# Kernel tuning notes

Hardware: AMD Instinct MI355X
Metric: run time of the kernel (lower is better)

The kernel has to match this reference:

```python
import jax, jax.numpy as jnp
import numpy as np

N, M, D = 20000, 16000, 128

def setup_inputs() -> dict:
    key = jax.random.key(0)
    ks = jax.random.split(key, 4)
    return {
        "clear_feature": jax.random.normal(ks[0], (N, D), dtype=jnp.float32),
        "rain_feature": jax.random.normal(ks[1], (M, D), dtype=jnp.float32),
        # torch nn.Linear weight layout: (out_features, in_features)
        "W1": jax.random.normal(ks[2], (D, 2 * D), dtype=jnp.float32) * 0.05,
        "b1": jnp.zeros((D,), dtype=jnp.float32),
        "W2": jax.random.normal(ks[3], (1, D), dtype=jnp.float32) * 0.05,
        "b2": jnp.zeros((1,), dtype=jnp.float32),
    }

def reference(clear_feature, rain_feature, W1, b1, W2, b2):
    # --- KNN alignment (k=1): argmin of squared Euclidean distance == cdist+topk(smallest) ---
    x2 = jnp.sum(clear_feature * clear_feature, axis=-1, keepdims=True)   # [N,1]
    y2 = jnp.sum(rain_feature * rain_feature, axis=-1)                    # [M]
    d2 = x2 + y2 - 2.0 * (clear_feature @ rain_feature.T)                 # [N,M]
    idx = jnp.argmin(d2, axis=-1)                                         # [N]
    aligned = rain_feature[idx]                                           # [N,D] gather
    # --- attention MLP: Linear(2D->D) + ReLU + Linear(D->1) + Sigmoid ---
    comb = jnp.concatenate([clear_feature, aligned], axis=-1)             # [N,2D]
    h = jax.nn.relu(comb @ W1.T + b1)                                     # [N,D]
    w = jax.nn.sigmoid(h @ W2.T + b2)                                     # [N,1]
    # --- gated fusion ---
    return w * clear_feature + (1.0 - w) * aligned
```

## Files before the change

### kernel.cpp

```cpp
#include <hip/hip_runtime.h>
#include <stdint.h>

#define NN 20000
#define MM 16000
#define DD 128
#define CT2 250
#define SPLITS 32
#define RB2 40

typedef unsigned long long u64;
typedef _Float16 f16x8 __attribute__((ext_vector_type(8)));
typedef float f32x16 __attribute__((ext_vector_type(16)));

__global__ void k_y2(const float* __restrict__ rain, float* __restrict__ y2) {
    int row = blockIdx.x * 4 + (threadIdx.x >> 6);
    int lane = threadIdx.x & 63;
    if (row >= MM) return;
    float2 v = ((const float2*)(rain + (size_t)row * DD))[lane];
    float s = v.x * v.x + v.y * v.y;
    #pragma unroll
    for (int off = 32; off > 0; off >>= 1) s += __shfl_down(s, off);
    if (lane == 0) y2[row] = s;
}

__global__ void k_split_B(const float* __restrict__ rain, _Float16* __restrict__ Bimg) {
    int id = blockIdx.x * 256 + threadIdx.x;
    if (id >= CT2 * 1024) return;
    int cl = id & 31;
    int cg = (id >> 5) & 1;
    int kp = (id >> 6) & 15;
    int tc = id >> 10;
    int row = tc * 64 + cg * 32 + cl;
    const float4* src = (const float4*)(rain + (size_t)row * DD + kp * 8);
    float4 v0 = src[0], v1 = src[1];
    float x[8] = {v0.x, v0.y, v0.z, v0.w, v1.x, v1.y, v1.z, v1.w};
    _Float16 hi[8], lo[8];
    #pragma unroll
    for (int j = 0; j < 8; ++j) {
        _Float16 h = (_Float16)x[j];
        hi[j] = h;
        lo[j] = (_Float16)(x[j] - (float)h);
    }
    int ks = kp >> 1, kh = kp & 1;
    int chunk = ((ks * 2 + cg) * 2 + kh) * 32 + cl;
    size_t base = (size_t)tc * 16384;
    *(f16x8*)(Bimg + base + (size_t)chunk * 8) = *(f16x8*)hi;
    *(f16x8*)(Bimg + base + 8192 + (size_t)chunk * 8) = *(f16x8*)lo;
}

__global__ void k_w1img(const float* __restrict__ W1, _Float16* __restrict__ W1img) {
    int id = blockIdx.x * 256 + threadIdx.x;
    if (id >= 4096) return;
    int cl = id & 31;
    int kh = (id >> 5) & 1;
    int cg = (id >> 6) & 3;
    int ks = id >> 8;
    int d = cg * 32 + cl;
    int k = ks * 16 + kh * 8;
    const float4* src = (const float4*)(W1 + (size_t)d * 256 + k);
    float4 v0 = src[0], v1 = src[1];
    float x[8] = {v0.x, v0.y, v0.z, v0.w, v1.x, v1.y, v1.z, v1.w};
    _Float16 h[8];
    #pragma unroll
    for (int j = 0; j < 8; ++j) h[j] = (_Float16)x[j];
    *(f16x8*)(W1img + (size_t)id * 8) = *(f16x8*)h;
}

__global__ __launch_bounds__(512, 2) void k_dist(
        const float* __restrict__ clear_f,
        const _Float16* __restrict__ Bimg, const float* __restrict__ y2,
        u64* __restrict__ keys2) {
    __shared__ _Float16 lds[3][16384];
    __shared__ float y2s[512];

    const int tid = threadIdx.x;
    const int w = tid >> 6, lane = tid & 63;
    const int l5 = lane >> 5, l31 = lane & 31;
    const int b = blockIdx.x;
    const int split = b & 31;
    const int n0 = (b >> 5) * 512;
    const int nt = (CT2 - split + SPLITS - 1) / SPLITS;

    #define STAGE(T, BUF) do {                                                 \
        const _Float16* gsrc_ = Bimg + (size_t)(T) * 16384;                    \
        _Float16* dst_ = &lds[BUF][0];                                         \
        _Pragma("unroll")                                                      \
        for (int n_ = 0; n_ < 4; ++n_) {                                       \
            int seg_ = w * 4 + n_;                                             \
            __builtin_amdgcn_global_load_lds(                                  \
                (const __attribute__((address_space(1))) unsigned int*)        \
                    (gsrc_ + (size_t)seg_ * 512 + (size_t)lane * 8),           \
                (__attribute__((address_space(3))) unsigned int*)              \
                    (dst_ + (size_t)seg_ * 512),                               \
                16, 0, 0);                                                     \
        }                                                                      \
    } while (0)

    STAGE(split, 0);
    if (nt > 1) STAGE(split + SPLITS, 1);

    for (int j = tid; j < nt * 64; j += 512) {
        int tt = j >> 6;
        int cc = j & 63;
        y2s[j] = y2[(split + tt * SPLITS) * 64 + cc];
    }

    f16x8 afh[2][8], afl[2][8];
    #pragma unroll
    for (int rb = 0; rb < 2; ++rb) {
        int r = n0 + w * 64 + rb * 32 + l31;
        if (r >= NN) r = NN - 1;
        const float* ap = clear_f + (size_t)r * DD + l5 * 8;
        #pragma unroll
        for (int ks = 0; ks < 8; ++ks) {
            float4 v0 = *(const float4*)(ap + ks * 16);
            float4 v1 = *(const float4*)(ap + ks * 16 + 4);
            float x[8] = {v0.x, v0.y, v0.z, v0.w, v1.x, v1.y, v1.z, v1.w};
            _Float16 hi[8], lo[8];
            #pragma unroll
            for (int j = 0; j < 8; ++j) {
                float s = -2.f * x[j];
                _Float16 h = (_Float16)s;
                hi[j] = h;
                lo[j] = (_Float16)(s - (float)h);
            }
            afh[rb][ks] = *(f16x8*)hi;
            afl[rb][ks] = *(f16x8*)lo;
        }
    }

    asm volatile("s_waitcnt lgkmcnt(0)" ::: "memory");

    float bestd[32];
    unsigned bits[4] = {0u, 0u, 0u, 0u};
    #pragma unroll
    for (int s = 0; s < 32; ++s) bestd[s] = 1e30f;

    int p = 0;
    for (int i = 0; i < nt; ++i) {
        if (i + 1 < nt) {
            asm volatile("s_waitcnt vmcnt(4)" ::: "memory");
        } else {
            asm volatile("s_waitcnt vmcnt(0)" ::: "memory");
        }
        __builtin_amdgcn_s_barrier();
        __builtin_amdgcn_sched_barrier(0);

        if (i + 2 < nt) {
            int p2 = p + 2; if (p2 >= 3) p2 -= 3;
            STAGE(split + (i + 2) * SPLITS, p2);
        }

        float y2v0 = y2s[i * 64 + l31];
        float y2v1 = y2s[i * 64 + 32 + l31];

        f32x16 acc00, acc01, acc10, acc11;
        #pragma unroll
        for (int e = 0; e < 16; ++e) {
            acc00[e] = y2v0; acc10[e] = y2v0;
            acc01[e] = y2v1; acc11[e] = y2v1;
        }

        const _Float16* lbuf = &lds[p][0];
        #pragma unroll
        for (int ks = 0; ks < 8; ++ks) {
            f16x8 bh0 = *(const f16x8*)(lbuf + (size_t)(ks * 2 + 0) * 512 + (size_t)lane * 8);
            f16x8 bh1 = *(const f16x8*)(lbuf + (size_t)(ks * 2 + 1) * 512 + (size_t)lane * 8);
            f16x8 bl0 = *(const f16x8*)(lbuf + 8192 + (size_t)(ks * 2 + 0) * 512 + (size_t)lane * 8);
            f16x8 bl1 = *(const f16x8*)(lbuf + 8192 + (size_t)(ks * 2 + 1) * 512 + (size_t)lane * 8);
            __builtin_amdgcn_s_setprio(1);
            acc00 = __builtin_amdgcn_mfma_f32_32x32x16_f16(afh[0][ks], bh0, acc00, 0, 0, 0);
            acc10 = __builtin_amdgcn_mfma_f32_32x32x16_f16(afh[1][ks], bh0, acc10, 0, 0, 0);
            acc01 = __builtin_amdgcn_mfma_f32_32x32x16_f16(afh[0][ks], bh1, acc01, 0, 0, 0);
            acc11 = __builtin_amdgcn_mfma_f32_32x32x16_f16(afh[1][ks], bh1, acc11, 0, 0, 0);
            acc00 = __builtin_amdgcn_mfma_f32_32x32x16_f16(afh[0][ks], bl0, acc00, 0, 0, 0);
            acc10 = __builtin_amdgcn_mfma_f32_32x32x16_f16(afh[1][ks], bl0, acc10, 0, 0, 0);
            acc01 = __builtin_amdgcn_mfma_f32_32x32x16_f16(afh[0][ks], bl1, acc01, 0, 0, 0);
            acc11 = __builtin_amdgcn_mfma_f32_32x32x16_f16(afh[1][ks], bl1, acc11, 0, 0, 0);
            acc00 = __builtin_amdgcn_mfma_f32_32x32x16_f16(afl[0][ks], bh0, acc00, 0, 0, 0);
            acc10 = __builtin_amdgcn_mfma_f32_32x32x16_f16(afl[1][ks], bh0, acc10, 0, 0, 0);
            acc01 = __builtin_amdgcn_mfma_f32_32x32x16_f16(afl[0][ks], bh1, acc01, 0, 0, 0);
            acc11 = __builtin_amdgcn_mfma_f32_32x32x16_f16(afl[1][ks], bh1, acc11, 0, 0, 0);
            __builtin_amdgcn_s_setprio(0);
        }

        const unsigned ibase = (unsigned)i << 1;
        #pragma unroll
        for (int e = 0; e < 16; ++e) {
            {
                float d0 = acc00[e], d1 = acc01[e];
                bool tk = d1 < d0;
                float dm = tk ? d1 : d0;
                int s = e, sh = 4 * (e & 7);
                bool up = dm < bestd[s];
                bestd[s] = up ? dm : bestd[s];
                unsigned nib = ibase | (unsigned)tk;
                bits[s >> 3] = up ? ((bits[s >> 3] & ~(15u << sh)) | (nib << sh))
                                  : bits[s >> 3];
            }
            {
                float d0 = acc10[e], d1 = acc11[e];
                bool tk = d1 < d0;
                float dm = tk ? d1 : d0;
                int s = 16 + e, sh = 4 * (s & 7);
                bool up = dm < bestd[s];
                bestd[s] = up ? dm : bestd[s];
                unsigned nib = ibase | (unsigned)tk;
                bits[s >> 3] = up ? ((bits[s >> 3] & ~(15u << sh)) | (nib << sh))
                                  : bits[s >> 3];
            }
        }

        ++p; if (p == 3) p = 0;
    }
    #undef STAGE

    #pragma unroll
    for (int s = 0; s < 32; ++s) {
        unsigned nib = (bits[s >> 3] >> (4 * (s & 7))) & 15u;
        int i4 = (int)(nib >> 1), cg = (int)(nib & 1);
        int col = (split + i4 * SPLITS) * 64 + cg * 32 + l31;
        unsigned u = __float_as_uint(bestd[s]);
        u = (u & 0x80000000u) ? ~u : (u | 0x80000000u);
        u64 key = ((u64)u << 32) | (unsigned)col;
        #pragma unroll
        for (int off = 1; off < 32; off <<= 1) {
            u64 o = __shfl_xor(key, off);
            if (o < key) key = o;
        }
        if (l31 == 0) {
            int e = s & 15, rb = s >> 4;
            int grow = n0 + w * 64 + rb * 32 + (e & 3) + 8 * (e >> 2) + 4 * l5;
            if (grow < NN) keys2[(size_t)grow * SPLITS + split] = key;
        }
    }
}

__global__ void k_reduce(const u64* __restrict__ keys2, int* __restrict__ idx) {
    int gid = blockIdx.x * 256 + threadIdx.x;
    int row = gid >> 5, j = gid & 31;
    if (row >= NN) return;
    u64 k = keys2[(size_t)row * SPLITS + j];
    #pragma unroll
    for (int off = 16; off > 0; off >>= 1) {
        u64 o = __shfl_xor(k, off);
        if (o < k) k = o;
    }
    if (j == 0) idx[row] = (int)(k & 0xffffffffu);
}

__global__ __launch_bounds__(64) void k_mlp(
        const float* __restrict__ clear_f, const float* __restrict__ rain_f,
        const _Float16* __restrict__ W1img, const float* __restrict__ b1,
        const float* __restrict__ W2, const float* __restrict__ b2,
        const int* __restrict__ idx, float* __restrict__ out) {
    const int lane = threadIdx.x;
    const int l5 = lane >> 5, l31 = lane & 31;
    const int n0 = blockIdx.x * 32;

    int n = n0 + l31;
    int nc = n < NN ? n : NN - 1;
    int rid = idx[nc];
    f16x8 af[16];
    #pragma unroll
    for (int ks = 0; ks < 16; ++ks) {
        int k0 = ks * 16 + l5 * 8;
        const float4* src = (k0 < 128)
            ? (const float4*)(clear_f + (size_t)nc * DD + k0)
            : (const float4*)(rain_f + (size_t)rid * DD + (k0 - 128));
        float4 v0 = src[0], v1 = src[1];
        float x[8] = {v0.x, v0.y, v0.z, v0.w, v1.x, v1.y, v1.z, v1.w};
        _Float16 h[8];
        #pragma unroll
        for (int j = 0; j < 8; ++j) h[j] = (_Float16)x[j];
        af[ks] = *(f16x8*)h;
    }

    f32x16 acc[4];
    #pragma unroll
    for (int cg = 0; cg < 4; ++cg)
        #pragma unroll
        for (int e = 0; e < 16; ++e) acc[cg][e] = 0.f;

    #pragma unroll
    for (int ks = 0; ks < 16; ++ks) {
        #pragma unroll
        for (int cg = 0; cg < 4; ++cg) {
            f16x8 bh = *(const f16x8*)(W1img +
                ((size_t)((ks * 4 + cg) * 2 + l5)) * 256 + (size_t)l31 * 8);
            acc[cg] = __builtin_amdgcn_mfma_f32_32x32x16_f16(af[ks], bh, acc[cg], 0, 0, 0);
        }
    }

    float b1v[4], w2v[4];
    #pragma unroll
    for (int cg = 0; cg < 4; ++cg) {
        b1v[cg] = b1[cg * 32 + l31];
        w2v[cg] = W2[cg * 32 + l31];
    }
    float b2v = b2[0];

    #pragma unroll
    for (int e = 0; e < 16; ++e) {
        float part = 0.f;
        #pragma unroll
        for (int cg = 0; cg < 4; ++cg) {
            float hv = acc[cg][e] + b1v[cg];
            hv = hv > 0.f ? hv : 0.f;
            part = fmaf(hv, w2v[cg], part);
        }
        #pragma unroll
        for (int off = 1; off < 32; off <<= 1) part += __shfl_xor(part, off);
        float s = part + b2v;
        float wv = 1.f / (1.f + expf(-s));
        int row = n0 + (e & 3) + 8 * (e >> 2) + 4 * l5;
        if (row < NN) {
            int rid2 = idx[row];
            float4 cv = *(const float4*)(clear_f + (size_t)row * DD + l31 * 4);
            float4 av = *(const float4*)(rain_f + (size_t)rid2 * DD + l31 * 4);
            float4 ov;
            ov.x = wv * cv.x + (1.f - wv) * av.x;
            ov.y = wv * cv.y + (1.f - wv) * av.y;
            ov.z = wv * cv.z + (1.f - wv) * av.z;
            ov.w = wv * cv.w + (1.f - wv) * av.w;
            *(float4*)(out + (size_t)row * DD + l31 * 4) = ov;
        }
    }
}

extern "C" void kernel_launch(void* const* d_in, const int* in_sizes, int n_in,
                              void* d_out, int out_size, void* d_ws, size_t ws_size,
                              hipStream_t stream) {
    const float* clear_f = (const float*)d_in[0];
    const float* rain_f = (const float*)d_in[1];
    const float* W1 = (const float*)d_in[2];
    const float* b1 = (const float*)d_in[3];
    const float* W2 = (const float*)d_in[4];
    const float* b2 = (const float*)d_in[5];
    float* out = (float*)d_out;

    char* ws = (char*)d_ws;
    u64* keys2 = (u64*)ws;
    int* idx = (int*)(ws + 5120000);
    float* y2 = (float*)(ws + 5200000);
    _Float16* Bimg = (_Float16*)(ws + 5264000);
    _Float16* W1img = (_Float16*)(ws + 13456000);

    k_y2<<<MM / 4, 256, 0, stream>>>(rain_f, y2);
    k_split_B<<<(CT2 * 1024 + 255) / 256, 256, 0, stream>>>(rain_f, Bimg);
    k_w1img<<<16, 256, 0, stream>>>(W1, W1img);
    k_dist<<<RB2 * SPLITS, 512, 0, stream>>>(clear_f, Bimg, y2, keys2);
    k_reduce<<<(NN * 32 + 255) / 256, 256, 0, stream>>>(keys2, idx);
    k_mlp<<<(NN + 31) / 32, 64, 0, stream>>>(clear_f, rain_f, W1img, b1, W2, b2, idx, out);
}
```

Baseline: 414.4 us.

## Shrink distance tile to 32x32 per wave with double-buffered LDS

Reworks the KNN distance kernel so each wave computes a 32-row by 32-column tile instead of 64x64. Blocks drop to 256 threads with 128 rows each, launched over many more row blocks. The B image is repacked into 32-column tiles, the triple-buffered async pipeline becomes a double buffer synchronised with __syncthreads, and the lo-correction term gets its own accumulator. The aim is more occupancy and more blocks in flight, at the cost of less register and LDS reuse per MFMA, a full barrier every iteration, and a dependent MFMA chain on the main accumulator.

After: 357.3 us. 13.8% less time.

```diff
diff --git a/kernel.cpp b/kernel.cpp
--- a/kernel.cpp
+++ b/kernel.cpp
@@ -4,9 +4,9 @@
 #define NN 20000
 #define MM 16000
 #define DD 128
-#define CT2 250
+#define CT 500
 #define SPLITS 32
-#define RB2 40
+#define RBG 157
 
 typedef unsigned long long u64;
 typedef _Float16 f16x8 __attribute__((ext_vector_type(8)));
@@ -25,13 +25,13 @@
 
 __global__ void k_split_B(const float* __restrict__ rain, _Float16* __restrict__ Bimg) {
     int id = blockIdx.x * 256 + threadIdx.x;
-    if (id >= CT2 * 1024) return;
+    if (id >= CT * 512) return;
     int cl = id & 31;
-    int cg = (id >> 5) & 1;
-    int kp = (id >> 6) & 15;
-    int tc = id >> 10;
-    int row = tc * 64 + cg * 32 + cl;
-    const float4* src = (const float4*)(rain + (size_t)row * DD + kp * 8);
+    int kh = (id >> 5) & 1;
+    int ks = (id >> 6) & 7;
+    int tc = id >> 9;
+    int m = tc * 32 + cl;
+    const float4* src = (const float4*)(rain + (size_t)m * DD + ks * 16 + kh * 8);
     float4 v0 = src[0], v1 = src[1];
     float x[8] = {v0.x, v0.y, v0.z, v0.w, v1.x, v1.y, v1.z, v1.w};
     _Float16 hi[8], lo[8];
@@ -41,11 +41,10 @@
         hi[j] = h;
         lo[j] = (_Float16)(x[j] - (float)h);
     }
-    int ks = kp >> 1, kh = kp & 1;
-    int chunk = ((ks * 2 + cg) * 2 + kh) * 32 + cl;
-    size_t base = (size_t)tc * 16384;
+    int chunk = (ks * 2 + kh) * 32 + cl;
+    size_t base = (size_t)tc * 8192;
     *(f16x8*)(Bimg + base + (size_t)chunk * 8) = *(f16x8*)hi;
-    *(f16x8*)(Bimg + base + 8192 + (size_t)chunk * 8) = *(f16x8*)lo;
+    *(f16x8*)(Bimg + base + 4096 + (size_t)chunk * 8) = *(f16x8*)lo;
 }
 
 __global__ void k_w1img(const float* __restrict__ W1, _Float16* __restrict__ W1img) {
@@ -66,11 +65,11 @@
     *(f16x8*)(W1img + (size_t)id * 8) = *(f16x8*)h;
 }
 
-__global__ __launch_bounds__(512, 2) void k_dist(
+__global__ __launch_bounds__(256, 3) void k_dist(
         const float* __restrict__ clear_f,
         const _Float16* __restrict__ Bimg, const float* __restrict__ y2,
         u64* __restrict__ keys2) {
-    __shared__ _Float16 lds[3][16384];
+    __shared__ _Float16 lds[2][8192];
     __shared__ float y2s[512];
 
     const int tid = threadIdx.x;
@@ -78,11 +77,11 @@
     const int l5 = lane >> 5, l31 = lane & 31;
     const int b = blockIdx.x;
     const int split = b & 31;
-    const int n0 = (b >> 5) * 512;
-    const int nt = (CT2 - split + SPLITS - 1) / SPLITS;
+    const int n0 = (b >> 5) * 128;
+    const int nt = (CT - split + SPLITS - 1) / SPLITS;
 
     #define STAGE(T, BUF) do {                                                 \
-        const _Float16* gsrc_ = Bimg + (size_t)(T) * 16384;                    \
+        const _Float16* gsrc_ = Bimg + (size_t)(T) * 8192;                     \
         _Float16* dst_ = &lds[BUF][0];                                         \
         _Pragma("unroll")                                                      \
         for (int n_ = 0; n_ < 4; ++n_) {                                       \
@@ -97,18 +96,16 @@
     } while (0)
 
     STAGE(split, 0);
-    if (nt > 1) STAGE(split + SPLITS, 1);
-
-    for (int j = tid; j < nt * 64; j += 512) {
-        int tt = j >> 6;
-        int cc = j & 63;
-        y2s[j] = y2[(split + tt * SPLITS) * 64 + cc];
-    }
-
-    f16x8 afh[2][8], afl[2][8];
-    #pragma unroll
-    for (int rb = 0; rb < 2; ++rb) {
-        int r = n0 + w * 64 + rb * 32 + l31;
+
+    for (int j = tid; j < nt * 32; j += 256) {
+        int tt = j >> 5;
+        int cc = j & 31;
+        y2s[j] = y2[(split + tt * SPLITS) * 32 + cc];
+    }
+
+    f16x8 afh[8], afl[8];
+    {
+        int r = n0 + w * 32 + l31;
         if (r >= NN) r = NN - 1;
         const float* ap = clear_f + (size_t)r * DD + l5 * 8;
         #pragma unroll
@@ -124,102 +121,60 @@
                 hi[j] = h;
                 lo[j] = (_Float16)(s - (float)h);
             }
-            afh[rb][ks] = *(f16x8*)hi;
-            afl[rb][ks] = *(f16x8*)lo;
-        }
-    }
-
-    asm volatile("s_waitcnt lgkmcnt(0)" ::: "memory");
-
-    float bestd[32];
-    unsigned bits[4] = {0u, 0u, 0u, 0u};
-    #pragma unroll
-    for (int s = 0; s < 32; ++s) bestd[s] = 1e30f;
+            afh[ks] = *(f16x8*)hi;
+            afl[ks] = *(f16x8*)lo;
+        }
+    }
+
+    __syncthreads();
+
+    float bestd[16];
+    unsigned bits[2] = {0u, 0u};
+    #pragma unroll
+    for (int s = 0; s < 16; ++s) bestd[s] = 1e30f;
 
     int p = 0;
     for (int i = 0; i < nt; ++i) {
-        if (i + 1 < nt) {
-            asm volatile("s_waitcnt vmcnt(4)" ::: "memory");
-        } else {
-            asm volatile("s_waitcnt vmcnt(0)" ::: "memory");
-        }
-        __builtin_amdgcn_s_barrier();
-        __builtin_amdgcn_sched_barrier(0);
-
-        if (i + 2 < nt) {
-            int p2 = p + 2; if (p2 >= 3) p2 -= 3;
-            STAGE(split + (i + 2) * SPLITS, p2);
-        }
-
-        float y2v0 = y2s[i * 64 + l31];
-        float y2v1 = y2s[i * 64 + 32 + l31];
-
-        f32x16 acc00, acc01, acc10, acc11;
+        if (i + 1 < nt) STAGE(split + (i + 1) * SPLITS, 1 - p);
+
+        float y2v = y2s[i * 32 + l31];
+
+        f32x16 accA, accB;
+        #pragma unroll
+        for (int e = 0; e < 16; ++e) { accA[e] = y2v; accB[e] = 0.f; }
+
+        const _Float16* lbuf = &lds[p][0];
+        #pragma unroll
+        for (int ks = 0; ks < 8; ++ks) {
+            f16x8 bh = *(const f16x8*)(lbuf + (size_t)ks * 512 + (size_t)lane * 8);
+            f16x8 bl = *(const f16x8*)(lbuf + 4096 + (size_t)ks * 512 + (size_t)lane * 8);
+            __builtin_amdgcn_s_setprio(1);
+            accA = __builtin_amdgcn_mfma_f32_32x32x16_f16(afh[ks], bh, accA, 0, 0, 0);
+            accB = __builtin_amdgcn_mfma_f32_32x32x16_f16(afl[ks], bh, accB, 0, 0, 0);
+            accA = __builtin_amdgcn_mfma_f32_32x32x16_f16(afh[ks], bl, accA, 0, 0, 0);
+            __builtin_amdgcn_s_setprio(0);
+        }
+
+        const unsigned nib = (unsigned)i;
         #pragma unroll
         for (int e = 0; e < 16; ++e) {
-            acc00[e] = y2v0; acc10[e] = y2v0;
-            acc01[e] = y2v1; acc11[e] = y2v1;
-        }
-
-        const _Float16* lbuf = &lds[p][0];
-        #pragma unroll
-        for (int ks = 0; ks < 8; ++ks) {
-            f16x8 bh0 = *(const f16x8*)(lbuf + (size_t)(ks * 2 + 0) * 512 + (size_t)lane * 8);
-            f16x8 bh1 = *(const f16x8*)(lbuf + (size_t)(ks * 2 + 1) * 512 + (size_t)lane * 8);
-            f16x8 bl0 = *(const f16x8*)(lbuf + 8192 + (size_t)(ks * 2 + 0) * 512 + (size_t)lane * 8);
-            f16x8 bl1 = *(const f16x8*)(lbuf + 8192 + (size_t)(ks * 2 + 1) * 512 + (size_t)lane * 8);
-            __builtin_amdgcn_s_setprio(1);
-            acc00 = __builtin_amdgcn_mfma_f32_32x32x16_f16(afh[0][ks], bh0, acc00, 0, 0, 0);
-            acc10 = __builtin_amdgcn_mfma_f32_32x32x16_f16(afh[1][ks], bh0, acc10, 0, 0, 0);
-            acc01 = __builtin_amdgcn_mfma_f32_32x32x16_f16(afh[0][ks], bh1, acc01, 0, 0, 0);
-            acc11 = __builtin_amdgcn_mfma_f32_32x32x16_f16(afh[1][ks], bh1, acc11, 0, 0, 0);
-            acc00 = __builtin_amdgcn_mfma_f32_32x32x16_f16(afh[0][ks], bl0, acc00, 0, 0, 0);
-            acc10 = __builtin_amdgcn_mfma_f32_32x32x16_f16(afh[1][ks], bl0, acc10, 0, 0, 0);
-            acc01 = __builtin_amdgcn_mfma_f32_32x32x16_f16(afh[0][ks], bl1, acc01, 0, 0, 0);
-            acc11 = __builtin_amdgcn_mfma_f32_32x32x16_f16(afh[1][ks], bl1, acc11, 0, 0, 0);
-            acc00 = __builtin_amdgcn_mfma_f32_32x32x16_f16(afl[0][ks], bh0, acc00, 0, 0, 0);
-            acc10 = __builtin_amdgcn_mfma_f32_32x32x16_f16(afl[1][ks], bh0, acc10, 0, 0, 0);
-            acc01 = __builtin_amdgcn_mfma_f32_32x32x16_f16(afl[0][ks], bh1, acc01, 0, 0, 0);
-            acc11 = __builtin_amdgcn_mfma_f32_32x32x16_f16(afl[1][ks], bh1, acc11, 0, 0, 0);
-            __builtin_amdgcn_s_setprio(0);
-        }
-
-        const unsigned ibase = (unsigned)i << 1;
-        #pragma unroll
-        for (int e = 0; e < 16; ++e) {
-            {
-                float d0 = acc00[e], d1 = acc01[e];
-                bool tk = d1 < d0;
-                float dm = tk ? d1 : d0;
-                int s = e, sh = 4 * (e & 7);
-                bool up = dm < bestd[s];
-                bestd[s] = up ? dm : bestd[s];
-                unsigned nib = ibase | (unsigned)tk;
-                bits[s >> 3] = up ? ((bits[s >> 3] & ~(15u << sh)) | (nib << sh))
-                                  : bits[s >> 3];
-            }
-            {
-                float d0 = acc10[e], d1 = acc11[e];
-                bool tk = d1 < d0;
-                float dm = tk ? d1 : d0;
-                int s = 16 + e, sh = 4 * (s & 7);
-                bool up = dm < bestd[s];
-                bestd[s] = up ? dm : bestd[s];
-                unsigned nib = ibase | (unsigned)tk;
-                bits[s >> 3] = up ? ((bits[s >> 3] & ~(15u << sh)) | (nib << sh))
-                                  : bits[s >> 3];
-            }
-        }
-
-        ++p; if (p == 3) p = 0;
+            float d = accA[e] + accB[e];
+            int sh = 4 * (e & 7);
+            bool up = d < bestd[e];
+            bestd[e] = up ? d : bestd[e];
+            bits[e >> 3] = up ? ((bits[e >> 3] & ~(15u << sh)) | (nib << sh))
+                              : bits[e >> 3];
+        }
+
+        __syncthreads();
+        p ^= 1;
     }
     #undef STAGE
 
     #pragma unroll
-    for (int s = 0; s < 32; ++s) {
+    for (int s = 0; s < 16; ++s) {
         unsigned nib = (bits[s >> 3] >> (4 * (s & 7))) & 15u;
-        int i4 = (int)(nib >> 1), cg = (int)(nib & 1);
-        int col = (split + i4 * SPLITS) * 64 + cg * 32 + l31;
+        int col = (split + (int)nib * SPLITS) * 32 + l31;
         unsigned u = __float_as_uint(bestd[s]);
         u = (u & 0x80000000u) ? ~u : (u | 0x80000000u);
         u64 key = ((u64)u << 32) | (unsigned)col;
@@ -229,8 +184,7 @@
             if (o < key) key = o;
         }
         if (l31 == 0) {
-            int e = s & 15, rb = s >> 4;
-            int grow = n0 + w * 64 + rb * 32 + (e & 3) + 8 * (e >> 2) + 4 * l5;
+            int grow = n0 + w * 32 + (s & 3) + 8 * (s >> 2) + 4 * l5;
             if (grow < NN) keys2[(size_t)grow * SPLITS + split] = key;
         }
     }
@@ -347,9 +301,9 @@
     _Float16* W1img = (_Float16*)(ws + 13456000);
 
     k_y2<<<MM / 4, 256, 0, stream>>>(rain_f, y2);
-    k_split_B<<<(CT2 * 1024 + 255) / 256, 256, 0, stream>>>(rain_f, Bimg);
+    k_split_B<<<(CT * 512 + 255) / 256, 256, 0, stream>>>(rain_f, Bimg);
     k_w1img<<<16, 256, 0, stream>>>(W1, W1img);
-    k_dist<<<RB2 * SPLITS, 512, 0, stream>>>(clear_f, Bimg, y2, keys2);
+    k_dist<<<RBG * SPLITS, 256, 0, stream>>>(clear_f, Bimg, y2, keys2);
     k_reduce<<<(NN * 32 + 255) / 256, 256, 0, stream>>>(keys2, idx);
     k_mlp<<<(NN + 31) / 32, 64, 0, stream>>>(clear_f, rain_f, W1img, b1, W2, b2, idx, out);
 }
```

## Fuse prep kernels, shrink dist blocks, software-pipeline argmin fold, fold reduce into MLP

Applied to the files above, without the earlier changes.

The three preprocessing kernels merge into one launch, and the separate reduce kernel is folded into the MLP kernel, which now min-reduces the split keys itself. The distance kernel drops from 512-thread blocks with triple buffering to 256-thread blocks with double buffering and more blocks. Its inner loop splits into two column halves so the argmin fold of one half can overlap the MFMAs of the other. This targets launch overhead and ALU/MFMA serialization, at the cost of a full __syncthreads per tile and less prefetch depth. The NN bound checks are also removed, relying on NN being divisible by 32.

Result: slower. 736.4 us (+77.7%).

```diff
diff --git a/kernel.cpp b/kernel.cpp
--- a/kernel.cpp
+++ b/kernel.cpp
@@ -6,71 +6,72 @@
 #define DD 128
 #define CT2 250
 #define SPLITS 32
-#define RB2 40
+#define RB 79
 
 typedef unsigned long long u64;
 typedef _Float16 f16x8 __attribute__((ext_vector_type(8)));
 typedef float f32x16 __attribute__((ext_vector_type(16)));
 
-__global__ void k_y2(const float* __restrict__ rain, float* __restrict__ y2) {
-    int row = blockIdx.x * 4 + (threadIdx.x >> 6);
-    int lane = threadIdx.x & 63;
-    if (row >= MM) return;
-    float2 v = ((const float2*)(rain + (size_t)row * DD))[lane];
-    float s = v.x * v.x + v.y * v.y;
-    #pragma unroll
-    for (int off = 32; off > 0; off >>= 1) s += __shfl_down(s, off);
-    if (lane == 0) y2[row] = s;
+__global__ void k_prep(const float* __restrict__ rain, const float* __restrict__ W1,
+                       float* __restrict__ y2, _Float16* __restrict__ Bimg,
+                       _Float16* __restrict__ W1img) {
+    const int bb = blockIdx.x;
+    const int tid = threadIdx.x;
+    if (bb < 4000) {
+        int row = bb * 4 + (tid >> 6);
+        int lane = tid & 63;
+        if (row >= MM) return;
+        float2 v = ((const float2*)(rain + (size_t)row * DD))[lane];
+        float s = v.x * v.x + v.y * v.y;
+        #pragma unroll
+        for (int off = 32; off > 0; off >>= 1) s += __shfl_down(s, off);
+        if (lane == 0) y2[row] = s;
+    } else if (bb < 5000) {
+        int id = (bb - 4000) * 256 + tid;
+        int cl = id & 31;
+        int cg = (id >> 5) & 1;
+        int kp = (id >> 6) & 15;
+        int tc = id >> 10;
+        int row = tc * 64 + cg * 32 + cl;
+        const float4* src = (const float4*)(rain + (size_t)row * DD + kp * 8);
+        float4 v0 = src[0], v1 = src[1];
+        float x[8] = {v0.x, v0.y, v0.z, v0.w, v1.x, v1.y, v1.z, v1.w};
+        _Float16 hi[8], lo[8];
+        #pragma unroll
+        for (int j = 0; j < 8; ++j) {
+            _Float16 h = (_Float16)x[j];
+            hi[j] = h;
+            lo[j] = (_Float16)(x[j] - (float)h);
+        }
+        int ks = kp >> 1, kh = kp & 1;
+        int chunk = ((ks * 2 + cg) * 2 + kh) * 32 + cl;
+        size_t base = (size_t)tc * 16384;
+        *(f16x8*)(Bimg + base + (size_t)chunk * 8) = *(f16x8*)hi;
+        *(f16x8*)(Bimg + base + 8192 + (size_t)chunk * 8) = *(f16x8*)lo;
+    } else {
+        int id = (bb - 5000) * 256 + tid;
+        if (id >= 4096) return;
+        int cl = id & 31;
+        int kh = (id >> 5) & 1;
+        int cg = (id >> 6) & 3;
+        int ks = id >> 8;
+        int d = cg * 32 + cl;
+        int k = ks * 16 + kh * 8;
+        const float4* src = (const float4*)(W1 + (size_t)d * 256 + k);
+        float4 v0 = src[0], v1 = src[1];
+        float x[8] = {v0.x, v0.y, v0.z, v0.w, v1.x, v1.y, v1.z, v1.w};
+        _Float16 h[8];
+        #pragma unroll
+        for (int j = 0; j < 8; ++j) h[j] = (_Float16)x[j];
+        *(f16x8*)(W1img + (size_t)id * 8) = *(f16x8*)h;
+    }
 }
 
-__global__ void k_split_B(const float* __restrict__ rain, _Float16* __restrict__ Bimg) {
-    int id = blockIdx.x * 256 + threadIdx.x;
-    if (id >= CT2 * 1024) return;
-    int cl = id & 31;
-    int cg = (id >> 5) & 1;
-    int kp = (id >> 6) & 15;
-    int tc = id >> 10;
-    int row = tc * 64 + cg * 32 + cl;
-    const float4* src = (const float4*)(rain + (size_t)row * DD + kp * 8);
-    float4 v0 = src[0], v1 = src[1];
-    float x[8] = {v0.x, v0.y, v0.z, v0.w, v1.x, v1.y, v1.z, v1.w};
-    _Float16 hi[8], lo[8];
-    #pragma unroll
-    for (int j = 0; j < 8; ++j) {
-        _Float16 h = (_Float16)x[j];
-        hi[j] = h;
-        lo[j] = (_Float16)(x[j] - (float)h);
-    }
-    int ks = kp >> 1, kh = kp & 1;
-    int chunk = ((ks * 2 + cg) * 2 + kh) * 32 + cl;
-    size_t base = (size_t)tc * 16384;
-    *(f16x8*)(Bimg + base + (size_t)chunk * 8) = *(f16x8*)hi;
-    *(f16x8*)(Bimg + base + 8192 + (size_t)chunk * 8) = *(f16x8*)lo;
-}
-
-__global__ void k_w1img(const float* __restrict__ W1, _Float16* __restrict__ W1img) {
-    int id = blockIdx.x * 256 + threadIdx.x;
-    if (id >= 4096) return;
-    int cl = id & 31;
-    int kh = (id >> 5) & 1;
-    int cg = (id >> 6) & 3;
-    int ks = id >> 8;
-    int d = cg * 32 + cl;
-    int k = ks * 16 + kh * 8;
-    const float4* src = (const float4*)(W1 + (size_t)d * 256 + k);
-    float4 v0 = src[0], v1 = src[1];
-    float x[8] = {v0.x, v0.y, v0.z, v0.w, v1.x, v1.y, v1.z, v1.w};
-    _Float16 h[8];
-    #pragma unroll
-    for (int j = 0; j < 8; ++j) h[j] = (_Float16)x[j];
-    *(f16x8*)(W1img + (size_t)id * 8) = *(f16x8*)h;
-}
-
-__global__ __launch_bounds__(512, 2) void k_dist(
+__global__ __launch_bounds__(256, 2) void k_dist(
         const float* __restrict__ clear_f,
         const _Float16* __restrict__ Bimg, const float* __restrict__ y2,
         u64* __restrict__ keys2) {
-    __shared__ _Float16 lds[3][16384];
+    __shared__ _Float16 lds[2][16384];
     __shared__ float y2s[512];
 
     const int tid = threadIdx.x;
@@ -78,15 +79,15 @@
     const int l5 = lane >> 5, l31 = lane & 31;
     const int b = blockIdx.x;
     const int split = b & 31;
-    const int n0 = (b >> 5) * 512;
+    const int n0 = (b >> 5) * 256;
     const int nt = (CT2 - split + SPLITS - 1) / SPLITS;
 
     #define STAGE(T, BUF) do {                                                 \
         const _Float16* gsrc_ = Bimg + (size_t)(T) * 16384;                    \
         _Float16* dst_ = &lds[BUF][0];                                         \
         _Pragma("unroll")                                                      \
-        for (int n_ = 0; n_ < 4; ++n_) {                                       \
-            int seg_ = w * 4 + n_;                                             \
+        for (int n_ = 0; n_ < 8; ++n_) {                                       \
+            int seg_ = w * 8 + n_;                                             \
             __builtin_amdgcn_global_load_lds(                                  \
                 (const __attribute__((address_space(1))) unsigned int*)        \
                     (gsrc_ + (size_t)seg_ * 512 + (size_t)lane * 8),           \
@@ -97,9 +98,8 @@
     } while (0)
 
     STAGE(split, 0);
-    if (nt > 1) STAGE(split + SPLITS, 1);
-
-    for (int j = tid; j < nt * 64; j += 512) {
+
+    for (int j = tid; j < nt * 64; j += 256) {
         int tt = j >> 6;
         int cc = j & 63;
         y2s[j] = y2[(split + tt * SPLITS) * 64 + cc];
@@ -129,90 +129,90 @@
         }
     }
 
-    asm volatile("s_waitcnt lgkmcnt(0)" ::: "memory");
+    __syncthreads();
 
     float bestd[32];
     unsigned bits[4] = {0u, 0u, 0u, 0u};
     #pragma unroll
     for (int s = 0; s < 32; ++s) bestd[s] = 1e30f;
 
+    #define FOLD(A0, A1, CG, IDX) do {                                         \
+        const unsigned nib_ = (((unsigned)(IDX)) << 1) | (unsigned)(CG);       \
+        _Pragma("unroll")                                                      \
+        for (int e_ = 0; e_ < 16; ++e_) {                                      \
+            {                                                                  \
+                float d_ = A0[e_];                                             \
+                int sh_ = 4 * (e_ & 7);                                        \
+                bool up_ = d_ < bestd[e_];                                     \
+                bestd[e_] = up_ ? d_ : bestd[e_];                              \
+                bits[e_ >> 3] = up_ ? ((bits[e_ >> 3] & ~(15u << sh_)) | (nib_ << sh_)) \
+                                    : bits[e_ >> 3];                           \
+            }                                                                  \
+            {                                                                  \
+                float d_ = A1[e_];                                             \
+                int s_ = 16 + e_, sh_ = 4 * (s_ & 7);                          \
+                bool up_ = d_ < bestd[s_];                                     \
+                bestd[s_] = up_ ? d_ : bestd[s_];                              \
+                bits[s_ >> 3] = up_ ? ((bits[s_ >> 3] & ~(15u << sh_)) | (nib_ << sh_)) \
+                                    : bits[s_ >> 3];                           \
+            }                                                                  \
+        }                                                                      \
+    } while (0)
+
+    f32x16 acc00, acc01, acc10, acc11;
+    #pragma unroll
+    for (int e = 0; e < 16; ++e) { acc01[e] = 1e30f; acc11[e] = 1e30f; }
+
     int p = 0;
     for (int i = 0; i < nt; ++i) {
-        if (i + 1 < nt) {
-            asm volatile("s_waitcnt vmcnt(4)" ::: "memory");
-        } else {
-            asm volatile("s_waitcnt vmcnt(0)" ::: "memory");
-        }
-        __builtin_amdgcn_s_barrier();
-        __builtin_amdgcn_sched_barrier(0);
-
-        if (i + 2 < nt) {
-            int p2 = p + 2; if (p2 >= 3) p2 -= 3;
-            STAGE(split + (i + 2) * SPLITS, p2);
-        }
+        if (i + 1 < nt) STAGE(split + (i + 1) * SPLITS, 1 - p);
 
         float y2v0 = y2s[i * 64 + l31];
         float y2v1 = y2s[i * 64 + 32 + l31];
 
-        f32x16 acc00, acc01, acc10, acc11;
-        #pragma unroll
-        for (int e = 0; e < 16; ++e) {
-            acc00[e] = y2v0; acc10[e] = y2v0;
-            acc01[e] = y2v1; acc11[e] = y2v1;
-        }
-
         const _Float16* lbuf = &lds[p][0];
+
+        #pragma unroll
+        for (int e = 0; e < 16; ++e) { acc00[e] = y2v0; acc10[e] = y2v0; }
         #pragma unroll
         for (int ks = 0; ks < 8; ++ks) {
             f16x8 bh0 = *(const f16x8*)(lbuf + (size_t)(ks * 2 + 0) * 512 + (size_t)lane * 8);
-            f16x8 bh1 = *(const f16x8*)(lbuf + (size_t)(ks * 2 + 1) * 512 + (size_t)lane * 8);
             f16x8 bl0 = *(const f16x8*)(lbuf + 8192 + (size_t)(ks * 2 + 0) * 512 + (size_t)lane * 8);
-            f16x8 bl1 = *(const f16x8*)(lbuf + 8192 + (size_t)(ks * 2 + 1) * 512 + (size_t)lane * 8);
             __builtin_amdgcn_s_setprio(1);
             acc00 = __builtin_amdgcn_mfma_f32_32x32x16_f16(afh[0][ks], bh0, acc00, 0, 0, 0);
             acc10 = __builtin_amdgcn_mfma_f32_32x32x16_f16(afh[1][ks], bh0, acc10, 0, 0, 0);
+            acc00 = __builtin_amdgcn_mfma_f32_32x32x16_f16(afl[0][ks], bh0, acc00, 0, 0, 0);
+            acc10 = __builtin_amdgcn_mfma_f32_32x32x16_f16(afl[1][ks], bh0, acc10, 0, 0, 0);
+            acc00 = __builtin_amdgcn_mfma_f32_32x32x16_f16(afh[0][ks], bl0, acc00, 0, 0, 0);
+            acc10 = __builtin_amdgcn_mfma_f32_32x32x16_f16(afh[1][ks], bl0, acc10, 0, 0, 0);
+            __builtin_amdgcn_s_setprio(0);
+        }
+
+        FOLD(acc01, acc11, 1, i - 1);
+
+        #pragma unroll
+        for (int e = 0; e < 16; ++e) { acc01[e] = y2v1; acc11[e] = y2v1; }
+        #pragma unroll
+        for (int ks = 0; ks < 8; ++ks) {
+            f16x8 bh1 = *(const f16x8*)(lbuf + (size_t)(ks * 2 + 1) * 512 + (size_t)lane * 8);
+            f16x8 bl1 = *(const f16x8*)(lbuf + 8192 + (size_t)(ks * 2 + 1) * 512 + (size_t)lane * 8);
+            __builtin_amdgcn_s_setprio(1);
             acc01 = __builtin_amdgcn_mfma_f32_32x32x16_f16(afh[0][ks], bh1, acc01, 0, 0, 0);
             acc11 = __builtin_amdgcn_mfma_f32_32x32x16_f16(afh[1][ks], bh1, acc11, 0, 0, 0);
-            acc00 = __builtin_amdgcn_mfma_f32_32x32x16_f16(afh[0][ks], bl0, acc00, 0, 0, 0);
-            acc10 = __builtin_amdgcn_mfma_f32_32x32x16_f16(afh[1][ks], bl0, acc10, 0, 0, 0);
+            acc01 = __builtin_amdgcn_mfma_f32_32x32x16_f16(afl[0][ks], bh1, acc01, 0, 0, 0);
+            acc11 = __builtin_amdgcn_mfma_f32_32x32x16_f16(afl[1][ks], bh1, acc11, 0, 0, 0);
             acc01 = __builtin_amdgcn_mfma_f32_32x32x16_f16(afh[0][ks], bl1, acc01, 0, 0, 0);
             acc11 = __builtin_amdgcn_mfma_f32_32x32x16_f16(afh[1][ks], bl1, acc11, 0, 0, 0);
-            acc00 = __builtin_amdgcn_mfma_f32_32x32x16_f16(afl[0][ks], bh0, acc00, 0, 0, 0);
-            acc10 = __builtin_amdgcn_mfma_f32_32x32x16_f16(afl[1][ks], bh0, acc10, 0, 0, 0);
-            acc01 = __builtin_amdgcn_mfma_f32_32x32x16_f16(afl[0][ks], bh1, acc01, 0, 0, 0);
-            acc11 = __builtin_amdgcn_mfma_f32_32x32x16_f16(afl[1][ks], bh1, acc11, 0, 0, 0);
             __builtin_amdgcn_s_setprio(0);
         }
 
-        const unsigned ibase = (unsigned)i << 1;
-        #pragma unroll
-        for (int e = 0; e < 16; ++e) {
-            {
-                float d0 = acc00[e], d1 = acc01[e];
-                bool tk = d1 < d0;
-                float dm = tk ? d1 : d0;
-                int s = e, sh = 4 * (e & 7);
-                bool up = dm < bestd[s];
-                bestd[s] = up ? dm : bestd[s];
-                unsigned nib = ibase | (unsigned)tk;
-                bits[s >> 3] = up ? ((bits[s >> 3] & ~(15u << sh)) | (nib << sh))
-                                  : bits[s >> 3];
-            }
-            {
-                float d0 = acc10[e], d1 = acc11[e];
-                bool tk = d1 < d0;
-                float dm = tk ? d1 : d0;
-                int s = 16 + e, sh = 4 * (s & 7);
-                bool up = dm < bestd[s];
-                bestd[s] = up ? dm : bestd[s];
-                unsigned nib = ibase | (unsigned)tk;
-                bits[s >> 3] = up ? ((bits[s >> 3] & ~(15u << sh)) | (nib << sh))
-                                  : bits[s >> 3];
-            }
-        }
-
-        ++p; if (p == 3) p = 0;
-    }
+        FOLD(acc00, acc10, 0, i);
+
+        __syncthreads();
+        p ^= 1;
+    }
+    FOLD(acc01, acc11, 1, nt - 1);
+    #undef FOLD
     #undef STAGE
 
     #pragma unroll
@@ -236,31 +236,34 @@
     }
 }
 
-__global__ void k_reduce(const u64* __restrict__ keys2, int* __restrict__ idx) {
-    int gid = blockIdx.x * 256 + threadIdx.x;
-    int row = gid >> 5, j = gid & 31;
-    if (row >= NN) return;
-    u64 k = keys2[(size_t)row * SPLITS + j];
-    #pragma unroll
-    for (int off = 16; off > 0; off >>= 1) {
-        u64 o = __shfl_xor(k, off);
-        if (o < k) k = o;
-    }
-    if (j == 0) idx[row] = (int)(k & 0xffffffffu);
-}
-
 __global__ __launch_bounds__(64) void k_mlp(
         const float* __restrict__ clear_f, const float* __restrict__ rain_f,
         const _Float16* __restrict__ W1img, const float* __restrict__ b1,
         const float* __restrict__ W2, const float* __restrict__ b2,
-        const int* __restrict__ idx, float* __restrict__ out) {
+        const u64* __restrict__ keys2, float* __restrict__ out) {
+    __shared__ int idxs[32];
+
     const int lane = threadIdx.x;
     const int l5 = lane >> 5, l31 = lane & 31;
     const int n0 = blockIdx.x * 32;
 
-    int n = n0 + l31;
-    int nc = n < NN ? n : NN - 1;
-    int rid = idx[nc];
+    {
+        int r = lane >> 1;
+        const u64* pk = keys2 + (size_t)(n0 + r) * SPLITS + (lane & 1) * 16;
+        u64 best = pk[0];
+        #pragma unroll
+        for (int t = 1; t < 16; ++t) {
+            u64 k2 = pk[t];
+            if (k2 < best) best = k2;
+        }
+        u64 o = __shfl_xor(best, 1);
+        if (o < best) best = o;
+        if ((lane & 1) == 0) idxs[r] = (int)(best & 0xffffffffu);
+    }
+    __syncthreads();
+
+    int nc = n0 + l31;
+    int rid = idxs[l31];
     f16x8 af[16];
     #pragma unroll
     for (int ks = 0; ks < 16; ++ks) {
@@ -314,17 +317,15 @@
         float s = part + b2v;
         float wv = 1.f / (1.f + expf(-s));
         int row = n0 + (e & 3) + 8 * (e >> 2) + 4 * l5;
-        if (row < NN) {
-            int rid2 = idx[row];
-            float4 cv = *(const float4*)(clear_f + (size_t)row * DD + l31 * 4);
-            float4 av = *(const float4*)(rain_f + (size_t)rid2 * DD + l31 * 4);
-            float4 ov;
-            ov.x = wv * cv.x + (1.f - wv) * av.x;
-            ov.y = wv * cv.y + (1.f - wv) * av.y;
-            ov.z = wv * cv.z + (1.f - wv) * av.z;
-            ov.w = wv * cv.w + (1.f - wv) * av.w;
-            *(float4*)(out + (size_t)row * DD + l31 * 4) = ov;
-        }
+        int rid2 = idxs[row - n0];
+        float4 cv = *(const float4*)(clear_f + (size_t)row * DD + l31 * 4);
+        float4 av = *(const float4*)(rain_f + (size_t)rid2 * DD + l31 * 4);
+        float4 ov;
+        ov.x = wv * cv.x + (1.f - wv) * av.x;
+        ov.y = wv * cv.y + (1.f - wv) * av.y;
+        ov.z = wv * cv.z + (1.f - wv) * av.z;
+        ov.w = wv * cv.w + (1.f - wv) * av.w;
+        *(float4*)(out + (size_t)row * DD + l31 * 4) = ov;
     }
 }
 
@@ -341,15 +342,11 @@
 
     char* ws = (char*)d_ws;
     u64* keys2 = (u64*)ws;
-    int* idx = (int*)(ws + 5120000);
-    float* y2 = (float*)(ws + 5200000);
-    _Float16* Bimg = (_Float16*)(ws + 5264000);
-    _Float16* W1img = (_Float16*)(ws + 13456000);
-
-    k_y2<<<MM / 4, 256, 0, stream>>>(rain_f, y2);
-    k_split_B<<<(CT2 * 1024 + 255) / 256, 256, 0, stream>>>(rain_f, Bimg);
-    k_w1img<<<16, 256, 0, stream>>>(W1, W1img);
-    k_dist<<<RB2 * SPLITS, 512, 0, stream>>>(clear_f, Bimg, y2, keys2);
-    k_reduce<<<(NN * 32 + 255) / 256, 256, 0, stream>>>(keys2, idx);
-    k_mlp<<<(NN + 31) / 32, 64, 0, stream>>>(clear_f, rain_f, W1img, b1, W2, b2, idx, out);
+    float* y2 = (float*)(ws + 5120000);
+    _Float16* Bimg = (_Float16*)(ws + 5184000);
+    _Float16* W1img = (_Float16*)(ws + 13376000);
+
+    k_prep<<<5016, 256, 0, stream>>>(rain_f, W1, y2, Bimg, W1img);
+    k_dist<<<RB * SPLITS, 256, 0, stream>>>(clear_f, Bimg, y2, keys2);
+    k_mlp<<<NN / 32, 64, 0, stream>>>(clear_f, rain_f, W1img, b1, W2, b2, keys2, out);
 }
```
